# Kernel tuning notes

Measured on AMD Instinct MI355X. Metric: run time of the kernel, lower is better.

The kernel has to match this reference:

```python
import jax, jax.numpy as jnp
import numpy as np

N_NODES = 10000
N_EDGES = 160000
DIM_IN = 32
DIM_OUT = 64
DIM_EDGE_HIDDEN = 128
BOND_FDIM = 13


def setup_inputs() -> dict:
    key = jax.random.key(0)
    ks = jax.random.split(key, 10)
    s = 0.1
    x = jax.random.normal(ks[0], (N_NODES, DIM_IN), dtype=jnp.float32)
    edge_index = jax.random.randint(ks[1], (2, N_EDGES), 0, N_NODES, dtype=jnp.int64)
    edge_attr = jax.random.uniform(ks[2], (N_EDGES, BOND_FDIM), dtype=jnp.float32)
    # edge-MLP params: BOND_FDIM -> hidden -> in*out
    W1 = jax.random.normal(ks[3], (BOND_FDIM, DIM_EDGE_HIDDEN), dtype=jnp.float32) * s
    b1 = jnp.zeros((DIM_EDGE_HIDDEN,), dtype=jnp.float32)
    W2 = jax.random.normal(ks[4], (DIM_EDGE_HIDDEN, DIM_IN * DIM_OUT), dtype=jnp.float32) * s
    b2 = jnp.zeros((DIM_IN * DIM_OUT,), dtype=jnp.float32)
    # NNConv root weight + bias
    root = jax.random.normal(ks[5], (DIM_IN, DIM_OUT), dtype=jnp.float32) * s
    bias = jnp.zeros((DIM_OUT,), dtype=jnp.float32)
    return {"x": x, "edge_index": edge_index, "edge_attr": edge_attr,
            "W1": W1, "b1": b1, "W2": W2, "b2": b2, "root": root, "bias": bias}


def reference(x, edge_index, edge_attr, W1, b1, W2, b2, root, bias):
    src, dst = edge_index[0], edge_index[1]  # PyG: row=source j, col=target i
    # edge MLP -> per-edge weight matrix [E, in, out]
    h = jax.nn.relu(edge_attr @ W1 + b1)
    w = (h @ W2 + b2).reshape(-1, DIM_IN, DIM_OUT)
    # gather source features, per-edge matmul -> messages [E, out]
    msg = jnp.einsum('ei,eio->eo', x[src], w)
    # scatter-add to target nodes
    agg = jax.ops.segment_sum(msg, dst, num_segments=N_NODES)
    out = agg + x @ root + bias
    return jax.nn.relu(out)
```

## Files before the change

### kernel.cpp

```cpp
#include <hip/hip_runtime.h>

#define N_NODES 10000
#define N_EDGES 160000
#define DIM_IN 32
#define DIM_OUT 64
#define DIM_HID 128
#define BOND 13
#define NB 16
#define NGROUPS (N_NODES / NB)
#define CAP 96

typedef _Float16 half2_t __attribute__((ext_vector_type(2)));
typedef _Float16 f16x8 __attribute__((ext_vector_type(8)));
typedef float f32x4 __attribute__((ext_vector_type(4)));
typedef unsigned int uint;

static __device__ __forceinline__ uint packh2(float a, float b) {
    half2_t h;
    h.x = (_Float16)a; h.y = (_Float16)b;
    return __builtin_bit_cast(uint, h);
}

static __device__ __forceinline__ int swz(int o, int kp) { return (o + kp) & 63; }

struct EScr {
    uint     eids[16];
    _Float16 ea16[16][32];
    _Float16 hbuf16[16][136];
};

__global__ void prep_kernel(const float* __restrict__ W2, uint4* __restrict__ W2p,
                            const float* __restrict__ W1, uint4* __restrict__ W1p,
                            const int* __restrict__ ei, int* __restrict__ cnt,
                            uint* __restrict__ es,
                            const float* __restrict__ x, const float* __restrict__ root,
                            const float* __restrict__ bias, float* __restrict__ out) {
    int idx = blockIdx.x * 256 + threadIdx.x;
    if (idx < 512 * 64) {
        int f = idx >> 6, lane = idx & 63;
        int k = f >> 2, of = f & 3;
        int q = lane >> 4, l15 = lane & 15;
        const float* base = W2 + k * 2048 + q * 512 + of * 16 + l15;
        uint u0 = packh2(base[0],   base[64]);
        uint u1 = packh2(base[128], base[192]);
        uint u2 = packh2(base[256], base[320]);
        uint u3 = packh2(base[384], base[448]);
        W2p[idx] = make_uint4(u0, u1, u2, u3);
    }
    if (idx < 512) {
        int nh = idx >> 6, lane = idx & 63;
        int quad = lane >> 4, l15 = lane & 15;
        int col = nh * 16 + l15;
        uint u[4];
#pragma unroll
        for (int jp = 0; jp < 4; ++jp) {
            int k0 = quad * 8 + 2 * jp, k1 = k0 + 1;
            float f0 = (k0 < BOND) ? W1[k0 * DIM_HID + col] : 0.f;
            float f1 = (k1 < BOND) ? W1[k1 * DIM_HID + col] : 0.f;
            u[jp] = packh2(f0, f1);
        }
        W1p[idx] = make_uint4(u[0], u[1], u[2], u[3]);
    }
    if (idx < N_NODES * DIM_OUT) {
        int n = idx >> 6, o = idx & 63;
        float r = bias[o];
        const float* xn = x + n * DIM_IN;
#pragma unroll 8
        for (int i = 0; i < DIM_IN; ++i) r += xn[i] * root[i * DIM_OUT + o];
        out[idx] = r;
    }
    if (idx < N_EDGES) {
        int src = ei[idx];
        int dst = ei[N_EDGES + idx];
        int slot = atomicAdd(&cnt[src], 1);
        if (slot < CAP)
            es[src * CAP + slot] = ((uint)dst << 18) | (uint)idx;
    }
}

__global__ __launch_bounds__(1024)
__attribute__((amdgpu_waves_per_eu(4, 4)))
void phase1_kernel(
    const float* __restrict__ x,
    const float* __restrict__ ea, const uint4* __restrict__ W1p,
    const float* __restrict__ b1, const uint4* __restrict__ W2p,
    const float* __restrict__ b2, const int* __restrict__ cnt,
    const uint* __restrict__ es, float* __restrict__ out)
{
    __shared__ uint  PhH[NB][DIM_HID / 4][DIM_OUT];
    __shared__ uint4 w1lds[8][64];

    const int t  = threadIdx.x;
    const int o  = t & 63;
    const int w  = t >> 6;
    const int n0 = blockIdx.x * NB;
    const int l15  = o & 15;
    const int quad = o >> 4;
    const int nd = w;

    if (t < 512) w1lds[t >> 6][t & 63] = W1p[t];

    f16x8 af;
    {
        uint ua[4];
        const float* xn8 = x + (long)(n0 + l15) * DIM_IN;
#pragma unroll
        for (int jj = 0; jj < 4; ++jj)
            ua[jj] = packh2(xn8[quad * 8 + 2 * jj], xn8[quad * 8 + 2 * jj + 1]);
        af = __builtin_bit_cast(f16x8, make_uint4(ua[0], ua[1], ua[2], ua[3]));
    }

    f16x8 pregf[16];
    const int of = w & 3;
    const int ks = w >> 2;
#pragma unroll
    for (int h = 0; h < 2; ++h) {
        const int oo = of * 16 + l15;
        const int kbase = h * 64 + ks * 16;
#pragma unroll 2
        for (int m = 0; m < 8; ++m) {
            const int k0 = kbase + 2 * m;
            const uint4 bu0 = W2p[(k0 * 4 + of) * 64 + o];
            const uint4 bu1 = W2p[((k0 + 1) * 4 + of) * 64 + o];
            f32x4 D0 = {0.f, 0.f, 0.f, 0.f};
            f32x4 D1 = {0.f, 0.f, 0.f, 0.f};
            D0 = __builtin_amdgcn_mfma_f32_16x16x32_f16(
                     af, __builtin_bit_cast(f16x8, bu0), D0, 0, 0, 0);
            D1 = __builtin_amdgcn_mfma_f32_16x16x32_f16(
                     af, __builtin_bit_cast(f16x8, bu1), D1, 0, 0, 0);
            const int kpg = (kbase >> 1) + m;
            const int kpl = kpg & 31;
            const int sc = swz(oo, kpg);
#pragma unroll
            for (int r = 0; r < 4; ++r)
                PhH[quad * 4 + r][kpl][sc] = packh2(D0[r], D1[r]);
        }
        __syncthreads();
#pragma unroll
        for (int nt = 0; nt < 4; ++nt)
#pragma unroll
            for (int kh = 0; kh < 2; ++kh) {
                const int kk = 2 * h + kh;
                const int col = nt * 16 + l15;
                const int kpl = kh * 16 + quad * 4;
                const int kpg = h * 32 + kpl;
                uint4 u;
                u.x = PhH[nd][kpl + 0][swz(col, kpg + 0)];
                u.y = PhH[nd][kpl + 1][swz(col, kpg + 1)];
                u.z = PhH[nd][kpl + 2][swz(col, kpg + 2)];
                u.w = PhH[nd][kpl + 3][swz(col, kpg + 3)];
                pregf[nt * 4 + kk] = __builtin_bit_cast(f16x8, u);
            }
        __syncthreads();
    }

    const int n = n0 + nd;

    float qv[4] = {0.f, 0.f, 0.f, 0.f};
    {
        const float* xn = x + (long)n * DIM_IN;
#pragma unroll 4
        for (int i = 0; i < DIM_IN; ++i) {
            float xv = xn[i];
#pragma unroll
            for (int nt = 0; nt < 4; ++nt)
                qv[nt] += xv * b2[i * DIM_OUT + nt * 16 + l15];
        }
    }

    float b1v[8];
#pragma unroll
    for (int nh = 0; nh < 8; ++nh) b1v[nh] = b1[nh * 16 + l15];

    const int start = n * CAP;
    int deg = cnt[n];
    deg = deg < CAP ? deg : CAP;

    EScr* S = (EScr*)((char*)&PhH[0][0][0] + nd * 8192);

    ((uint4*)S->ea16)[o] = make_uint4(0u, 0u, 0u, 0u);
    __builtin_amdgcn_wave_barrier();

    const int ntiles = (deg + 15) >> 4;
#pragma unroll 1
    for (int tb = 0; tb < ntiles; ++tb) {
        const int tilebase = tb * 16;
        const int tcnt = (deg - tilebase < 16) ? (deg - tilebase) : 16;
        __builtin_amdgcn_wave_barrier();
        if (o < tcnt)
            S->eids[o] = es[start + tilebase + o];
        __builtin_amdgcn_wave_barrier();
        if (l15 < BOND) {
#pragma unroll
            for (int r = 0; r < 4; ++r) {
                int p = quad + 4 * r;
                if (p < tcnt) {
                    float v = ea[(long)(S->eids[p] & 0x3FFFFu) * BOND + l15];
                    S->ea16[p][l15] = (_Float16)v;
                }
            }
        }
        __builtin_amdgcn_wave_barrier();
        uint woff = 0;
        asm volatile("" : "+v"(woff));
        const int wo = (o + (int)woff) & 63;
        const f16x8 aef = *(const f16x8*)&S->ea16[l15][quad * 8];
#pragma unroll
        for (int nh = 0; nh < 8; ++nh) {
            const f16x8 wf = __builtin_bit_cast(f16x8, w1lds[nh][wo]);
            f32x4 hacc = {0.f, 0.f, 0.f, 0.f};
            hacc = __builtin_amdgcn_mfma_f32_16x16x32_f16(aef, wf, hacc, 0, 0, 0);
#pragma unroll
            for (int r = 0; r < 4; ++r) {
                float hv = hacc[r] + b1v[nh];
                S->hbuf16[quad * 4 + r][nh * 16 + l15] =
                    (_Float16)(hv > 0.f ? hv : 0.f);
            }
        }
        __builtin_amdgcn_wave_barrier();
        f16x8 hf[4];
#pragma unroll
        for (int kk = 0; kk < 4; ++kk)
            hf[kk] = *(const f16x8*)&S->hbuf16[l15][kk * 32 + quad * 8];
        uint pk[4];
#pragma unroll
        for (int r = 0; r < 4; ++r)
            pk[r] = S->eids[quad * 4 + r];
#pragma unroll
        for (int nt = 0; nt < 4; ++nt) {
            f32x4 acc = {0.f, 0.f, 0.f, 0.f};
#pragma unroll
            for (int kk = 0; kk < 4; ++kk)
                acc = __builtin_amdgcn_mfma_f32_16x16x32_f16(
                          hf[kk], pregf[nt * 4 + kk], acc, 0, 0, 0);
#pragma unroll
            for (int r = 0; r < 4; ++r) {
                if (quad * 4 + r < tcnt)
                    atomicAdd(&out[(long)(pk[r] >> 18) * DIM_OUT + nt * 16 + l15],
                              acc[r] + qv[nt]);
            }
        }
    }
}

__global__ __launch_bounds__(256) void relu_kernel(float* __restrict__ out) {
    int idx = blockIdx.x * 256 + threadIdx.x;
    if (idx < N_NODES * DIM_OUT) {
        float v = out[idx];
        out[idx] = v > 0.f ? v : 0.f;
    }
}


extern "C" void kernel_launch(void* const* d_in, const int* in_sizes, int n_in,
                              void* d_out, int out_size, void* d_ws, size_t ws_size,
                              hipStream_t stream) {
    const float* x    = (const float*)d_in[0];
    const int*   ei   = (const int*)d_in[1];
    const float* ea   = (const float*)d_in[2];
    const float* W1   = (const float*)d_in[3];
    const float* b1   = (const float*)d_in[4];
    const float* W2   = (const float*)d_in[5];
    const float* b2   = (const float*)d_in[6];
    const float* root = (const float*)d_in[7];
    const float* bias = (const float*)d_in[8];
    float* out = (float*)d_out;
    char* ws = (char*)d_ws;

    int*   cnt = (int*)(ws + 0);
    uint*  es  = (uint*)(ws + 40064);
    uint4* W2p = (uint4*)(ws + 3880064);
    uint4* W1p = (uint4*)(ws + 4404352);

    hipMemsetAsync(cnt, 0, 40064, stream);
    prep_kernel<<<2500, 256, 0, stream>>>(W2, W2p, W1, W1p, ei, cnt, es,
                                          x, root, bias, out);
    phase1_kernel<<<NGROUPS, 1024, 0, stream>>>(x, ea, W1p, b1, W2p, b2,
                                                cnt, es, out);
    relu_kernel<<<2500, 256, 0, stream>>>(out);
}
```

Measured before the change: 170.8 us.

## Prefetch next tile's edge ids and edge attributes into registers

```diff
diff --git a/kernel.cpp b/kernel.cpp
--- a/kernel.cpp
+++ b/kernel.cpp
@@ -24,7 +24,6 @@
 static __device__ __forceinline__ int swz(int o, int kp) { return (o + kp) & 63; }
 
 struct EScr {
-    uint     eids[16];
     _Float16 ea16[16][32];
     _Float16 hbuf16[16][136];
 };
@@ -97,8 +96,14 @@
     const int l15  = o & 15;
     const int quad = o >> 4;
     const int nd = w;
+    const int n  = n0 + nd;
 
     if (t < 512) w1lds[t >> 6][t & 63] = W1p[t];
+
+    const int start = n * CAP;
+    int deg = cnt[n];
+    uint pk = 0;
+    if (o < 16) pk = es[start + o];
 
     f16x8 af;
     {
@@ -108,6 +113,20 @@
         for (int jj = 0; jj < 4; ++jj)
             ua[jj] = packh2(xn8[quad * 8 + 2 * jj], xn8[quad * 8 + 2 * jj + 1]);
         af = __builtin_bit_cast(f16x8, make_uint4(ua[0], ua[1], ua[2], ua[3]));
+    }
+
+    deg = deg < CAP ? deg : CAP;
+    float eav[4];
+    {
+        const int tcnt0 = deg < 16 ? deg : 16;
+#pragma unroll
+        for (int r = 0; r < 4; ++r) {
+            const int p = quad + 4 * r;
+            const uint epk = __shfl(pk, p);
+            eav[r] = 0.f;
+            if (p < tcnt0 && l15 < BOND)
+                eav[r] = ea[(long)(epk & 0x3FFFFu) * BOND + l15];
+        }
     }
 
     f16x8 pregf[16];
@@ -154,8 +173,6 @@
         __syncthreads();
     }
 
-    const int n = n0 + nd;
-
     float qv[4] = {0.f, 0.f, 0.f, 0.f};
     {
         const float* xn = x + (long)n * DIM_IN;
@@ -172,10 +189,6 @@
 #pragma unroll
     for (int nh = 0; nh < 8; ++nh) b1v[nh] = b1[nh * 16 + l15];
 
-    const int start = n * CAP;
-    int deg = cnt[n];
-    deg = deg < CAP ? deg : CAP;
-
     EScr* S = (EScr*)((char*)&PhH[0][0][0] + nd * 8192);
 
     ((uint4*)S->ea16)[o] = make_uint4(0u, 0u, 0u, 0u);
@@ -187,20 +200,31 @@
         const int tilebase = tb * 16;
         const int tcnt = (deg - tilebase < 16) ? (deg - tilebase) : 16;
         __builtin_amdgcn_wave_barrier();
-        if (o < tcnt)
-            S->eids[o] = es[start + tilebase + o];
+        if (l15 < BOND) {
+#pragma unroll
+            for (int r = 0; r < 4; ++r) {
+                const int p = quad + 4 * r;
+                if (p < tcnt) S->ea16[p][l15] = (_Float16)eav[r];
+            }
+        }
         __builtin_amdgcn_wave_barrier();
-        if (l15 < BOND) {
+        const uint pkc = pk;
+
+        uint pk2 = 0;
+        float eav2[4] = {0.f, 0.f, 0.f, 0.f};
+        const int tb2 = tilebase + 16;
+        if (tb2 < deg) {
+            const int tcnt2 = (deg - tb2 < 16) ? (deg - tb2) : 16;
+            if (o < 16) pk2 = es[start + tb2 + o];
 #pragma unroll
             for (int r = 0; r < 4; ++r) {
-                int p = quad + 4 * r;
-                if (p < tcnt) {
-                    float v = ea[(long)(S->eids[p] & 0x3FFFFu) * BOND + l15];
-                    S->ea16[p][l15] = (_Float16)v;
-                }
-            }
-        }
-        __builtin_amdgcn_wave_barrier();
+                const int p = quad + 4 * r;
+                const uint epk = __shfl(pk2, p);
+                if (p < tcnt2 && l15 < BOND)
+                    eav2[r] = ea[(long)(epk & 0x3FFFFu) * BOND + l15];
+            }
+        }
+
         uint woff = 0;
         asm volatile("" : "+v"(woff));
         const int wo = (o + (int)woff) & 63;
@@ -222,10 +246,6 @@
 #pragma unroll
         for (int kk = 0; kk < 4; ++kk)
             hf[kk] = *(const f16x8*)&S->hbuf16[l15][kk * 32 + quad * 8];
-        uint pk[4];
-#pragma unroll
-        for (int r = 0; r < 4; ++r)
-            pk[r] = S->eids[quad * 4 + r];
 #pragma unroll
         for (int nt = 0; nt < 4; ++nt) {
             f32x4 acc = {0.f, 0.f, 0.f, 0.f};
@@ -235,11 +255,16 @@
                           hf[kk], pregf[nt * 4 + kk], acc, 0, 0, 0);
 #pragma unroll
             for (int r = 0; r < 4; ++r) {
-                if (quad * 4 + r < tcnt)
-                    atomicAdd(&out[(long)(pk[r] >> 18) * DIM_OUT + nt * 16 + l15],
+                const int p = quad * 4 + r;
+                const uint dpk = __shfl(pkc, p);
+                if (p < tcnt)
+                    atomicAdd(&out[(long)(dpk >> 18) * DIM_OUT + nt * 16 + l15],
                               acc[r] + qv[nt]);
             }
         }
+        pk = pk2;
+#pragma unroll
+        for (int r = 0; r < 4; ++r) eav[r] = eav2[r];
     }
 }
 
```

After: 171.0 us (median of 2 runs). Within noise of the previous version (+0.2%).
